# Performance work log

Measured on AMD Instinct MI355X. Metric: run time of the kernel, lower is better.

The kernel has to match this reference:

```python
import jax, jax.numpy as jnp
import numpy as np
import math

N, LQ, DIM = 4, 1000, 256
HEADS, DHEAD, DEPTH = 8, 32, 2
LVLS, NPTS, MLP = 5, 4, 512
SCALE = DHEAD ** -0.5
SHAPES = np.array([[128, 128], [64, 64], [32, 32], [16, 16], [8, 8]], np.int32)
AREAS = SHAPES[:, 0] * SHAPES[:, 1]
STARTS = np.concatenate([[0], np.cumsum(AREAS)[:-1]]).astype(np.int32)
LIN = int(AREAS.sum())


def _ln(x, g, b):
    m = jnp.mean(x, -1, keepdims=True)
    v = jnp.var(x, -1, keepdims=True)
    return (x - m) * jax.lax.rsqrt(v + 1e-5) * g + b


def _gelu(x):  # tanh-approx GELU exactly as the torch module
    c = math.sqrt(2.0 / math.pi)
    return 0.5 * x * (1.0 + jnp.tanh(c * (x + 0.044715 * x ** 3)))


def _ms_deform(value, shapes, starts, loc, aw):
    # value [N,Lin,H,D]; loc [N,Lq,H,L,P,2] normalized to [0,1]; aw [N,Lq,H,L,P]
    n, lq, h, L, p, _ = loc.shape
    d = value.shape[-1]
    ni = jnp.arange(n)[:, None, None, None]
    hi = jnp.arange(h)[None, None, :, None]
    out = jnp.zeros((n, lq, h, d), value.dtype)
    for l in range(L):  # fixed small pyramid depth
        Hl, Wl = int(shapes[l, 0]), int(shapes[l, 1])
        s = int(starts[l])
        v = value[:, s:s + Hl * Wl].reshape(n, Hl, Wl, h, d)
        gx = loc[:, :, :, l, :, 0] * Wl - 0.5  # [N,Lq,H,P]
        gy = loc[:, :, :, l, :, 1] * Hl - 0.5
        x0 = jnp.floor(gx); y0 = jnp.floor(gy)
        lx = gx - x0; ly = gy - y0
        x0i = x0.astype(jnp.int32); y0i = y0.astype(jnp.int32)
        def corner(yi, xi):
            ok = ((yi >= 0) & (yi < Hl) & (xi >= 0) & (xi < Wl)).astype(value.dtype)
            g = v[ni, jnp.clip(yi, 0, Hl - 1), jnp.clip(xi, 0, Wl - 1), hi]  # [N,Lq,H,P,D]
            return g * ok[..., None]
        samp = (corner(y0i, x0i) * ((1 - ly) * (1 - lx))[..., None]
                + corner(y0i, x0i + 1) * ((1 - ly) * lx)[..., None]
                + corner(y0i + 1, x0i) * (ly * (1 - lx))[..., None]
                + corner(y0i + 1, x0i + 1) * (ly * lx)[..., None])
        out = out + jnp.einsum('nqhp,nqhpd->nqhd', aw[:, :, :, l], samp)
    return out.reshape(n, lq, h * d)


def _forward(x, src, center_pos, pos_w, pos_b, ln1_g, ln1_b, qkv_w, out_w, out_b,
             ln2_g, ln2_b, off_w, off_b, aw_w, aw_b, val_w, val_b, op_w, op_b,
             ln3_g, ln3_b, ff_w1, ff_b1, ff_w2, ff_b2, spatial_shapes, level_start_index):
    shapes = np.asarray(spatial_shapes)
    starts = np.asarray(level_start_index)
    n, lq, dim = x.shape
    pe = center_pos @ pos_w + pos_b                                   # pos_embedding(center_pos)
    ref = jnp.broadcast_to(center_pos[:, :, None, :], (n, lq, LVLS, 2))
    onorm = jnp.asarray(np.stack([shapes[:, 1], shapes[:, 0]], -1), x.dtype)  # [L,2] = (W,H)
    for i in range(DEPTH):
        # --- self-attention: PreNorm(x + pe) ---
        xn = _ln(x + pe, ln1_g[i], ln1_b[i])
        qkv = xn @ qkv_w[i]
        q, k, v = jnp.split(qkv, 3, axis=-1)
        q = q.reshape(n, lq, HEADS, DHEAD).transpose(0, 2, 1, 3)
        k = k.reshape(n, lq, HEADS, DHEAD).transpose(0, 2, 1, 3)
        v = v.reshape(n, lq, HEADS, DHEAD).transpose(0, 2, 1, 3)
        att = jax.nn.softmax(jnp.einsum('nhid,nhjd->nhij', q, k) * SCALE, axis=-1)
        o = jnp.einsum('nhij,nhjd->nhid', att, v).transpose(0, 2, 1, 3).reshape(n, lq, HEADS * DHEAD)
        x = x + o @ out_w[i] + out_b[i]
        # --- deformable cross-attention: PreNorm_CA norms query and src with same LN ---
        xn = _ln(x, ln2_g[i], ln2_b[i])
        srcn = _ln(src, ln2_g[i], ln2_b[i])
        query = xn + pe
        value = (srcn @ val_w[i] + val_b[i]).reshape(n, -1, HEADS, DHEAD)
        off = (query @ off_w[i] + off_b[i]).reshape(n, lq, HEADS, LVLS, NPTS, 2)
        aw = jax.nn.softmax((query @ aw_w[i] + aw_b[i]).reshape(n, lq, HEADS, LVLS * NPTS), axis=-1)
        aw = aw.reshape(n, lq, HEADS, LVLS, NPTS)
        loc = ref[:, :, None, :, None, :] + off / onorm[None, None, None, :, None, :]
        o = _ms_deform(value, shapes, starts, loc, aw)
        x = x + o @ op_w[i] + op_b[i]
        # --- feedforward: PreNorm ---
        xn = _ln(x, ln3_g[i], ln3_b[i])
        x = x + _gelu(xn @ ff_w1[i] + ff_b1[i]) @ ff_w2[i] + ff_b2[i]
    return x


def setup_inputs() -> dict:
    key = jax.random.key(0)
    ks = iter(jax.random.split(key, 64))
    r = lambda sh, s=0.02: jax.random.normal(next(ks), sh, jnp.float32) * s
    # sampling_offsets bias grid init (as in MSDeformAttn._reset_parameters)
    thetas = np.arange(HEADS) * (2.0 * math.pi / HEADS)
    grid = np.stack([np.cos(thetas), np.sin(thetas)], -1)
    grid = grid / np.abs(grid).max(-1, keepdims=True)
    grid = np.tile(grid[:, None, None, :], (1, LVLS, NPTS, 1)) * (np.arange(NPTS) + 1)[None, None, :, None]
    off_b = jnp.tile(jnp.asarray(grid.reshape(-1), jnp.float32)[None], (DEPTH, 1))
    return dict(
        x=jax.random.normal(next(ks), (N, LQ, DIM), jnp.float32),
        src=jax.random.normal(next(ks), (N, LIN, DIM), jnp.float32),
        center_pos=jax.random.uniform(next(ks), (N, LQ, 2), jnp.float32),
        spatial_shapes=jnp.asarray(SHAPES),
        level_start_index=jnp.asarray(STARTS),
        pos_w=r((2, DIM), 0.5), pos_b=jnp.zeros((DIM,), jnp.float32),
        ln1_g=jnp.ones((DEPTH, DIM), jnp.float32), ln1_b=jnp.zeros((DEPTH, DIM), jnp.float32),
        qkv_w=r((DEPTH, DIM, 3 * HEADS * DHEAD)),
        out_w=r((DEPTH, HEADS * DHEAD, DIM)), out_b=jnp.zeros((DEPTH, DIM), jnp.float32),
        ln2_g=jnp.ones((DEPTH, DIM), jnp.float32), ln2_b=jnp.zeros((DEPTH, DIM), jnp.float32),
        off_w=r((DEPTH, DIM, HEADS * LVLS * NPTS * 2)), off_b=off_b,
        aw_w=r((DEPTH, DIM, HEADS * LVLS * NPTS)), aw_b=jnp.zeros((DEPTH, HEADS * LVLS * NPTS), jnp.float32),
        val_w=r((DEPTH, DIM, HEADS * DHEAD)), val_b=jnp.zeros((DEPTH, HEADS * DHEAD), jnp.float32),
        op_w=r((DEPTH, HEADS * DHEAD, DIM)), op_b=jnp.zeros((DEPTH, DIM), jnp.float32),
        ln3_g=jnp.ones((DEPTH, DIM), jnp.float32), ln3_b=jnp.zeros((DEPTH, DIM), jnp.float32),
        ff_w1=r((DEPTH, DIM, MLP)), ff_b1=jnp.zeros((DEPTH, MLP), jnp.float32),
        ff_w2=r((DEPTH, MLP, DIM)), ff_b2=jnp.zeros((DEPTH, DIM), jnp.float32),
    )


def reference(x, src, center_pos, spatial_shapes, level_start_index, pos_w, pos_b,
              ln1_g, ln1_b, qkv_w, out_w, out_b, ln2_g, ln2_b, off_w, off_b,
              aw_w, aw_b, val_w, val_b, op_w, op_b, ln3_g, ln3_b,
              ff_w1, ff_b1, ff_w2, ff_b2):
    return _forward(x, src, center_pos, pos_w, pos_b, ln1_g, ln1_b, qkv_w, out_w, out_b,
                    ln2_g, ln2_b, off_w, off_b, aw_w, aw_b, val_w, val_b, op_w, op_b,
                    ln3_g, ln3_b, ff_w1, ff_b1, ff_w2, ff_b2, spatial_shapes, level_start_index)
```

## Files before the change

kernel.cpp:

```cpp
#include <hip/hip_runtime.h>
#include <hip/hip_bf16.h>
#include <math.h>

#define DIM 256
#define NB 4
#define LQ 1000
#define MLPD 512
#define LIN 21824
#define ROWS_X 4000
#define ROWS_SRC 87296
#define ATT_SCALE 0.17677669529663687f
#define LDK 72
#define VLAYER ((size_t)ROWS_SRC*256)

typedef __hip_bfloat16 bf16;
typedef __attribute__((ext_vector_type(8))) short short8;
typedef __attribute__((ext_vector_type(4))) float floatx4;

__device__ __forceinline__ float rdv(const void* p, int f, size_t i){
    if (f) return ((const float*)p)[i];
    unsigned u = ((unsigned)((const unsigned short*)p)[i]) << 16;
    union { unsigned u; float f; } c; c.u = u; return c.f;
}
__device__ __forceinline__ short f2bs(float v){
    bf16 h = __float2bfloat16(v);
    return *reinterpret_cast<short*>(&h);
}
__device__ __forceinline__ float bs2f(short s){
    union { unsigned u; float f; } c; c.u = ((unsigned)(unsigned short)s) << 16; return c.f;
}

__global__ void detect_kernel(const void* __restrict__ x, int* __restrict__ flag){
    const unsigned short* u = (const unsigned short*)x;
    int t = threadIdx.x;
    bool hit = false;
    #pragma unroll
    for (int k = 0; k < 4; ++k) {
        unsigned short b = u[(t*4 + k)*2];
        union { unsigned u; float f; } c; c.u = ((unsigned)b) << 16;
        if (!(fabsf(c.f) <= 1000.f)) hit = true;
    }
    unsigned long long m = __ballot(hit);
    __shared__ unsigned long long red[4];
    if ((t & 63) == 0) red[t >> 6] = m;
    __syncthreads();
    if (t == 0) flag[0] = ((red[0]|red[1]|red[2]|red[3]) != 0ULL) ? 1 : 0;
}

struct PrepTab { const void* src[15]; float* dst[17]; int n[17]; int bs[18]; };
__global__ void prep_kernel(PrepTab t, const void* __restrict__ offb,
                            const void* __restrict__ awb, const void* __restrict__ pw,
                            const void* __restrict__ pb, const void* __restrict__ cp,
                            const int* __restrict__ flag){
    int f = flag[0];
    int bid = blockIdx.x;
    int j = 0;
    #pragma unroll 1
    while (bid >= t.bs[j+1]) ++j;
    int i = (bid - t.bs[j])*256 + threadIdx.x;
    if (i >= t.n[j]) return;
    if (j < 15) {
        t.dst[j][i] = t.src[j] ? rdv(t.src[j], f, i) : 0.f;
    } else if (j == 15) {
        int layer = i / 480, idx = i - layer*480;
        float v = (idx < 320) ? rdv(offb, f, (size_t)layer*320 + idx)
                              : rdv(awb,  f, (size_t)layer*160 + idx - 320);
        t.dst[15][i] = v;
    } else {
        int row = i >> 8, c = i & 255;
        float cx = rdv(cp, f, (size_t)row*2), cy = rdv(cp, f, (size_t)row*2 + 1);
        t.dst[16][i] = cx*rdv(pw, f, c) + cy*rdv(pw, f, DIM + c) + rdv(pb, f, c);
    }
}

struct WT { const void* src[8]; short* dst[8]; const float* scl[8];
            int K[8]; int N[8]; int ld[8]; int ro[8]; };
__global__ void wtransall_kernel(WT t, const int* __restrict__ flag){
    int j = blockIdx.z >> 1, b = blockIdx.z & 1;
    int K = t.K[j], N = t.N[j];
    int k0 = blockIdx.x*32, n0 = blockIdx.y*32;
    if (k0 >= K || n0 >= N) return;
    int f = flag[0];
    __shared__ float tt[32][33];
    int tx = threadIdx.x & 31, ty = threadIdx.x >> 5;
    size_t base = (size_t)b * K * N;
    for (int i = ty; i < 32; i += 8) {
        int k = k0 + i, n = n0 + tx;
        tt[i][tx] = (k < K && n < N) ? rdv(t.src[j], f, base + (size_t)k*N + n) : 0.f;
    }
    __syncthreads();
    int ld = t.ld[j], ro = t.ro[j];
    const float* sc = t.scl[j];
    for (int i = ty; i < 32; i += 8) {
        int n = n0 + i, k = k0 + tx;
        if (n < N && k < K) {
            float v = tt[tx][i];
            if (sc) v *= sc[(size_t)b*K + k];
            t.dst[j][(size_t)b*ld*K + (size_t)(ro+n)*K + k] = f2bs(v);
        }
    }
}

struct BFT { const void* W[3]; const float* bv[3]; const float* base[3];
             float* dst[3]; int N[3]; };
__global__ __launch_bounds__(256) void biasfold_kernel(BFT t, const int* __restrict__ flag){
    int f = flag[0];
    int x = blockIdx.x, b = blockIdx.y;
    int j, n;
    if (x < 768)       { j = 0; n = x; }
    else if (x < 1280) { j = 1; n = x - 768; }
    else               { j = 2; n = x - 1280; }
    int N = t.N[j];
    int k = threadIdx.x;
    float part = t.bv[j][(size_t)b*256 + k] *
                 rdv(t.W[j], f, (size_t)b*256*N + (size_t)k*N + n);
    #pragma unroll
    for (int o = 32; o; o >>= 1) part += __shfl_xor(part, o, 64);
    __shared__ float red[4];
    int wave = k >> 6, lane = k & 63;
    if (lane == 0) red[wave] = part;
    __syncthreads();
    if (k == 0) {
        float s = red[0] + red[1] + red[2] + red[3];
        if (t.base[j]) s += t.base[j][(size_t)b*N + n];
        t.dst[j][(size_t)b*N + n] = s;
    }
}

__global__ __launch_bounds__(256) void statsconvx_kernel(const void* __restrict__ src,
        const void* __restrict__ x, const float* __restrict__ pe,
        const int* __restrict__ flag, bf16* __restrict__ srcn,
        float* __restrict__ xf, float2* __restrict__ st, bf16* __restrict__ xab){
    int f = flag[0];
    int wave = threadIdx.x >> 6, lane = threadIdx.x & 63;
    int bid = blockIdx.x;
    if (bid < ROWS_SRC/4) {
        int row = bid*4 + wave;
        float v0, v1, v2, v3;
        if (f) {
            float4 xx = *(const float4*)((const float*)src + (size_t)row*DIM + lane*4);
            v0 = xx.x; v1 = xx.y; v2 = xx.z; v3 = xx.w;
        } else {
            ushort4 u = *(const ushort4*)((const unsigned short*)src + (size_t)row*DIM + lane*4);
            v0 = bs2f((short)u.x); v1 = bs2f((short)u.y);
            v2 = bs2f((short)u.z); v3 = bs2f((short)u.w);
        }
        float s  = v0 + v1 + v2 + v3;
        float s2 = v0*v0 + v1*v1 + v2*v2 + v3*v3;
        #pragma unroll
        for (int o = 32; o; o >>= 1) {
            s  += __shfl_xor(s,  o, 64);
            s2 += __shfl_xor(s2, o, 64);
        }
        float mean = s * (1.f/DIM);
        float rstd = rsqrtf(s2 * (1.f/DIM) - mean*mean + 1e-5f);
        ushort4 o4;
        o4.x = (unsigned short)f2bs((v0-mean)*rstd);
        o4.y = (unsigned short)f2bs((v1-mean)*rstd);
        o4.z = (unsigned short)f2bs((v2-mean)*rstd);
        o4.w = (unsigned short)f2bs((v3-mean)*rstd);
        *(ushort4*)((unsigned short*)srcn + (size_t)row*DIM + lane*4) = o4;
    } else {
        int row = (bid - ROWS_SRC/4)*4 + wave;
        float4 v;
        if (f) v = *(const float4*)((const float*)x + (size_t)row*DIM + lane*4);
        else {
            ushort4 u = *(const ushort4*)((const unsigned short*)x + (size_t)row*DIM + lane*4);
            v = make_float4(bs2f((short)u.x), bs2f((short)u.y), bs2f((short)u.z), bs2f((short)u.w));
        }
        *(float4*)(xf + (size_t)row*DIM + lane*4) = v;
        float4 p = *(const float4*)(pe + (size_t)row*DIM + lane*4);
        float a0 = v.x+p.x, a1 = v.y+p.y, a2 = v.z+p.z, a3 = v.w+p.w;
        float s  = a0+a1+a2+a3;
        float s2 = a0*a0+a1*a1+a2*a2+a3*a3;
        #pragma unroll
        for (int o = 32; o; o >>= 1) {
            s  += __shfl_xor(s,  o, 64);
            s2 += __shfl_xor(s2, o, 64);
        }
        if (lane == 0) st[row] = make_float2(s, s2);
        float mean = s * (1.f/DIM);
        float rstd = rsqrtf(s2 * (1.f/DIM) - mean*mean + 1e-5f);
        ushort4 o4;
        o4.x = (unsigned short)f2bs((a0-mean)*rstd);
        o4.y = (unsigned short)f2bs((a1-mean)*rstd);
        o4.z = (unsigned short)f2bs((a2-mean)*rstd);
        o4.w = (unsigned short)f2bs((a3-mean)*rstd);
        *(ushort4*)((unsigned short*)xab + (size_t)row*DIM + lane*4) = o4;
    }
}

__global__ __launch_bounds__(256) void xnorm_kernel(const float* __restrict__ a,
        const float* __restrict__ pre, const float* __restrict__ post,
        const float2* __restrict__ sums, const float* __restrict__ g,
        const float* __restrict__ b, bf16* __restrict__ out){
    int wave = threadIdx.x >> 6, lane = threadIdx.x & 63;
    int row = blockIdx.x*4 + wave;
    float4 x = *(const float4*)(a + (size_t)row*DIM + lane*4);
    if (pre) {
        float4 p = *(const float4*)(pre + (size_t)row*DIM + lane*4);
        x.x += p.x; x.y += p.y; x.z += p.z; x.w += p.w;
    }
    float2 st = sums[row];
    float mean = st.x * (1.f/256.f);
    float rstd = rsqrtf(st.y*(1.f/256.f) - mean*mean + 1e-5f);
    float v0 = (x.x-mean)*rstd, v1 = (x.y-mean)*rstd;
    float v2 = (x.z-mean)*rstd, v3 = (x.w-mean)*rstd;
    if (g) {
        int c = lane*4;
        float4 gv = *(const float4*)(g + c);
        float4 bv = *(const float4*)(b + c);
        v0 = v0*gv.x + bv.x; v1 = v1*gv.y + bv.y;
        v2 = v2*gv.z + bv.z; v3 = v3*gv.w + bv.w;
    }
    if (post) {
        float4 p = *(const float4*)(post + (size_t)row*DIM + lane*4);
        v0 += p.x; v1 += p.y; v2 += p.z; v3 += p.w;
    }
    ushort4 o4;
    o4.x = (unsigned short)f2bs(v0); o4.y = (unsigned short)f2bs(v1);
    o4.z = (unsigned short)f2bs(v2); o4.w = (unsigned short)f2bs(v3);
    *(ushort4*)((unsigned short*)out + (size_t)row*DIM + lane*4) = o4;
}

__global__ __launch_bounds__(256) void mgemm_kernel(
    const short* __restrict__ A, const short* __restrict__ Wt,
    const float* __restrict__ bias, const float* __restrict__ res,
    void* __restrict__ Cout, int M, int K, int N, int act, int cbf,
    float2* __restrict__ statacc, const float* __restrict__ sepe,
    void* __restrict__ fin, const int* __restrict__ flag){
    __shared__ short As[64*LDK];
    __shared__ short Bs[64*LDK];
    int tid = threadIdx.x;
    int wave = tid >> 6, lane = tid & 63;
    int wm = wave >> 1, wn = wave & 1;
    int quad = lane >> 4, l16 = lane & 15;
    int row0 = blockIdx.x*64, col0 = blockIdx.y*64;
    floatx4 acc[2][2];
    #pragma unroll
    for (int i = 0; i < 2; ++i)
        #pragma unroll
        for (int j = 0; j < 2; ++j)
            acc[i][j] = (floatx4){0.f,0.f,0.f,0.f};

    int r  = tid >> 2;
    int kc = (tid & 3) * 16;
    int gr = row0 + r;
    int gc = col0 + r;
    const short8 z8 = {0,0,0,0,0,0,0,0};

    short8 ra0, ra1, rb0, rb1;
    if (gr < M) {
        const short8* p = (const short8*)(A + (size_t)gr*K + kc);
        ra0 = p[0]; ra1 = p[1];
    }
    if (gc < N) {
        const short8* p = (const short8*)(Wt + (size_t)gc*K + kc);
        rb0 = p[0]; rb1 = p[1];
    }

    for (int k0 = 0; k0 < K; k0 += 64) {
        short8 a0 = z8, a1 = z8;
        if (gr < M) { a0 = ra0; a1 = ra1; }
        *(short8*)&As[r*LDK + kc]     = a0;
        *(short8*)&As[r*LDK + kc + 8] = a1;
        short8 b0 = z8, b1 = z8;
        if (gc < N) { b0 = rb0; b1 = rb1; }
        *(short8*)&Bs[r*LDK + kc]     = b0;
        *(short8*)&Bs[r*LDK + kc + 8] = b1;
        int kn = k0 + 64;
        if (kn < K) {
            if (gr < M) {
                const short8* p = (const short8*)(A + (size_t)gr*K + kn + kc);
                ra0 = p[0]; ra1 = p[1];
            }
            if (gc < N) {
                const short8* p = (const short8*)(Wt + (size_t)gc*K + kn + kc);
                rb0 = p[0]; rb1 = p[1];
            }
        }
        __syncthreads();
        #pragma unroll
        for (int kb = 0; kb < 64; kb += 32) {
            short8 af[2], bfr[2];
            #pragma unroll
            for (int mi = 0; mi < 2; ++mi)
                af[mi] = *(const short8*)&As[(wm*32 + mi*16 + l16)*LDK + kb + quad*8];
            #pragma unroll
            for (int ni = 0; ni < 2; ++ni)
                bfr[ni] = *(const short8*)&Bs[(wn*32 + ni*16 + l16)*LDK + kb + quad*8];
            #pragma unroll
            for (int mi = 0; mi < 2; ++mi)
                #pragma unroll
                for (int ni = 0; ni < 2; ++ni)
                    acc[mi][ni] = __builtin_amdgcn_mfma_f32_16x16x32_bf16(
                        af[mi], bfr[ni], acc[mi][ni], 0, 0, 0);
        }
        __syncthreads();
    }
    float vout[2][2][4];
    #pragma unroll
    for (int mi = 0; mi < 2; ++mi) {
        int rbase = row0 + wm*32 + mi*16 + quad*4;
        #pragma unroll
        for (int ni = 0; ni < 2; ++ni) {
            int c = col0 + wn*32 + ni*16 + l16;
            #pragma unroll
            for (int r2 = 0; r2 < 4; ++r2) {
                int rr = rbase + r2;
                float v = 0.f;
                if (c < N && rr < M) {
                    v = acc[mi][ni][r2];
                    if (bias) v += bias[c];
                    if (act) {
                        float z = fminf(1.5957691216057308f*(v + 0.044715f*v*v*v), 60.f);
                        float e = __expf(z);
                        v = v * e / (e + 1.f);
                    }
                    if (res) v += res[(size_t)rr*N + c];
                }
                vout[mi][ni][r2] = v;
            }
        }
    }
    int fflag = 0;
    if (fin) fflag = flag[0];
    #pragma unroll
    for (int mi = 0; mi < 2; ++mi) {
        int rbase = row0 + wm*32 + mi*16 + quad*4;
        #pragma unroll
        for (int ni = 0; ni < 2; ++ni) {
            int c = col0 + wn*32 + ni*16 + l16;
            if (c >= N) continue;
            #pragma unroll
            for (int r2 = 0; r2 < 4; ++r2) {
                int rr = rbase + r2;
                if (rr >= M) continue;
                float v = vout[mi][ni][r2];
                if (fin) {
                    float w = isfinite(v) ? v : 0.f;
                    if (fflag) ((float*)fin)[(size_t)rr*N + c] = w;
                    else       ((bf16*)fin)[(size_t)rr*N + c] = __float2bfloat16(w);
                } else if (cbf) ((bf16*)Cout)[(size_t)rr*N + c] = __float2bfloat16(v);
                else            ((float*)Cout)[(size_t)rr*N + c] = v;
            }
        }
    }
    if (statacc) {
        #pragma unroll
        for (int mi = 0; mi < 2; ++mi) {
            int rbase = row0 + wm*32 + mi*16 + quad*4;
            #pragma unroll
            for (int r2 = 0; r2 < 4; ++r2) {
                int rr = rbase + r2;
                float sv = 0.f, sq = 0.f;
                #pragma unroll
                for (int ni = 0; ni < 2; ++ni) {
                    int c = col0 + wn*32 + ni*16 + l16;
                    float v = vout[mi][ni][r2];
                    if (sepe && rr < M) v += sepe[(size_t)rr*256 + c];
                    sv += v; sq += v*v;
                }
                #pragma unroll
                for (int o = 1; o < 16; o <<= 1) {
                    sv += __shfl_xor(sv, o, 64);
                    sq += __shfl_xor(sq, o, 64);
                }
                if (l16 == 0 && rr < M) {
                    atomicAdd(&statacc[rr].x, sv);
                    atomicAdd(&statacc[rr].y, sq);
                }
            }
        }
    }
}

__global__ __launch_bounds__(256) void mgemm128_kernel(
    const short* __restrict__ A, const short* __restrict__ Wt,
    const float* __restrict__ bias, bf16* __restrict__ valall){
    const int K = 256;
    __shared__ short lds[2*128*LDK];
    short* As = lds;
    short* Bs = lds + 128*LDK;
    int tid = threadIdx.x;
    int wave = tid >> 6, lane = tid & 63;
    int wm = wave >> 1, wn = wave & 1;
    int quad = lane >> 4, l16 = lane & 15;
    int bid = blockIdx.x;
    int panel, col;
    if (bid < 2720) {
        int g = bid >> 5, w = bid & 31;
        panel = g*8 + (w & 7);
        col = w >> 3;
    } else {
        int idx = bid - 2720;
        panel = 680 + (idx >> 2);
        col = idx & 3;
    }
    int row0 = panel*128, col0 = col*128;
    floatx4 acc[4][4];
    #pragma unroll
    for (int i = 0; i < 4; ++i)
        #pragma unroll
        for (int j = 0; j < 4; ++j)
            acc[i][j] = (floatx4){0.f,0.f,0.f,0.f};

    short8 pa[2][2], pb2[2][2];
    #pragma unroll
    for (int i = 0; i < 2; ++i) {
        int idx = tid + i*256;
        int rr = idx >> 2, kk = (idx & 3)*16;
        const short8* p = (const short8*)(A + (size_t)(row0+rr)*K + kk);
        pa[i][0] = p[0]; pa[i][1] = p[1];
        const short8* pb = (const short8*)(Wt + (size_t)(col0+rr)*K + kk);
        pb2[i][0] = pb[0]; pb2[i][1] = pb[1];
    }
    for (int k0 = 0; k0 < K; k0 += 64) {
        #pragma unroll
        for (int i = 0; i < 2; ++i) {
            int idx = tid + i*256;
            int rr = idx >> 2, kk = (idx & 3)*16;
            *(short8*)&As[rr*LDK + kk]     = pa[i][0];
            *(short8*)&As[rr*LDK + kk + 8] = pa[i][1];
            *(short8*)&Bs[rr*LDK + kk]     = pb2[i][0];
            *(short8*)&Bs[rr*LDK + kk + 8] = pb2[i][1];
        }
        int kn = k0 + 64;
        if (kn < K) {
            #pragma unroll
            for (int i = 0; i < 2; ++i) {
                int idx = tid + i*256;
                int rr = idx >> 2, kk = (idx & 3)*16;
                const short8* p = (const short8*)(A + (size_t)(row0+rr)*K + kn + kk);
                pa[i][0] = p[0]; pa[i][1] = p[1];
                const short8* pb = (const short8*)(Wt + (size_t)(col0+rr)*K + kn + kk);
                pb2[i][0] = pb[0]; pb2[i][1] = pb[1];
            }
        }
        __syncthreads();
        #pragma unroll
        for (int kb = 0; kb < 64; kb += 32) {
            short8 af[4], bfr[4];
            #pragma unroll
            for (int mi = 0; mi < 4; ++mi)
                af[mi] = *(const short8*)&As[(wm*64 + mi*16 + l16)*LDK + kb + quad*8];
            #pragma unroll
            for (int ni = 0; ni < 4; ++ni)
                bfr[ni] = *(const short8*)&Bs[(wn*64 + ni*16 + l16)*LDK + kb + quad*8];
            #pragma unroll
            for (int mi = 0; mi < 4; ++mi)
                #pragma unroll
                for (int ni = 0; ni < 4; ++ni)
                    acc[mi][ni] = __builtin_amdgcn_mfma_f32_16x16x32_bf16(
                        af[mi], bfr[ni], acc[mi][ni], 0, 0, 0);
        }
        __syncthreads();
    }
    short* Cs = lds;
    #pragma unroll
    for (int mi = 0; mi < 4; ++mi) {
        int lr = wm*64 + mi*16 + quad*4;
        #pragma unroll
        for (int ni = 0; ni < 4; ++ni) {
            int lc = wn*64 + ni*16 + l16;
            float bv = bias[col0 + lc];
            #pragma unroll
            for (int r2 = 0; r2 < 4; ++r2)
                Cs[(lr + r2)*136 + lc] = f2bs(acc[mi][ni][r2] + bv);
        }
    }
    __syncthreads();
    #pragma unroll
    for (int g = 0; g < 4; ++g) {
        int cbase = col0 + g*32;
        int l = cbase >> 8, h = (cbase & 255) >> 5;
        #pragma unroll
        for (int p = 0; p < 2; ++p) {
            int idx = p*256 + tid;
            int rr2 = idx >> 2;
            int dc = (idx & 3) * 8;
            short8 v = *(const short8*)&Cs[rr2*136 + g*32 + dc];
            int grr = row0 + rr2;
            unsigned n = (unsigned)grr / (unsigned)LIN;
            int pos = grr - (int)n*LIN;
            *(short8*)((short*)valall + (size_t)l*VLAYER
                       + ((size_t)(n*8+h)*LIN + pos)*32 + dc) = v;
        }
    }
}

__global__ __launch_bounds__(256) void fattn_kernel(const short* __restrict__ qkv,
                                                    bf16* __restrict__ out){
    int nh = blockIdx.y;
    int n = nh >> 3, h = nh & 7;
    int q0 = blockIdx.x * 64;
    __shared__ short Ks[64*40];
    __shared__ short VsT[32*72];
    __shared__ short Ps[64*72];
    int tid = threadIdx.x;
    int wave = tid >> 6, lane = tid & 63;
    int quad = lane >> 4, l16 = lane & 15;
    int r = tid >> 2, c8 = (tid & 3) * 8;
    const short8 z8 = {0,0,0,0,0,0,0,0};

    short8 qf = z8;
    {
        int gq = q0 + wave*16 + l16;
        if (gq < LQ) {
            short8 s = *(const short8*)(qkv + ((size_t)(n*LQ+gq))*768 + h*32 + quad*8);
            #pragma unroll
            for (int j = 0; j < 8; ++j) qf[j] = f2bs(bs2f(s[j]) * ATT_SCALE);
        }
    }
    floatx4 acc[2];
    acc[0] = (floatx4){0.f,0.f,0.f,0.f};
    acc[1] = (floatx4){0.f,0.f,0.f,0.f};
    float m[4], lsum[4];
    #pragma unroll
    for (int i = 0; i < 4; ++i) { m[i] = -3.0e38f; lsum[i] = 0.f; }

    short8 kvp = z8, vvp = z8;
    if (r < LQ) {
        const short* rp = qkv + ((size_t)(n*LQ+r))*768;
        kvp = *(const short8*)(rp + 256 + h*32 + c8);
        vvp = *(const short8*)(rp + 512 + h*32 + c8);
    }
    for (int k0 = 0; k0 < LQ; k0 += 64) {
        *(short8*)&Ks[r*40 + c8] = kvp;
        #pragma unroll
        for (int j = 0; j < 8; ++j) VsT[(c8+j)*72 + r] = vvp[j];
        short8 kvn = z8, vvn = z8;
        if (k0 + 64 < LQ) {
            int gk = k0 + 64 + r;
            if (gk < LQ) {
                const short* rp = qkv + ((size_t)(n*LQ+gk))*768;
                kvn = *(const short8*)(rp + 256 + h*32 + c8);
                vvn = *(const short8*)(rp + 512 + h*32 + c8);
            }
        }
        __syncthreads();
        floatx4 s4[4];
        #pragma unroll
        for (int kg = 0; kg < 4; ++kg) {
            short8 bfr = *(const short8*)&Ks[(kg*16 + l16)*40 + quad*8];
            s4[kg] = __builtin_amdgcn_mfma_f32_16x16x32_bf16(
                qf, bfr, (floatx4){0.f,0.f,0.f,0.f}, 0, 0, 0);
        }
        if (k0 + 64 > LQ) {
            #pragma unroll
            for (int kg = 0; kg < 4; ++kg)
                if (k0 + kg*16 + l16 >= LQ)
                    s4[kg] = (floatx4){-3.0e38f,-3.0e38f,-3.0e38f,-3.0e38f};
        }
        float fac[4], psum[4];
        #pragma unroll
        for (int r2 = 0; r2 < 4; ++r2) {
            float v = fmaxf(fmaxf(s4[0][r2], s4[1][r2]), fmaxf(s4[2][r2], s4[3][r2]));
            v = fmaxf(v, __shfl_xor(v, 1, 64));
            v = fmaxf(v, __shfl_xor(v, 2, 64));
            v = fmaxf(v, __shfl_xor(v, 4, 64));
            v = fmaxf(v, __shfl_xor(v, 8, 64));
            float mn = fmaxf(m[r2], v);
            fac[r2] = __expf(m[r2] - mn);
            m[r2] = mn;
            psum[r2] = 0.f;
        }
        #pragma unroll
        for (int kg = 0; kg < 4; ++kg)
            #pragma unroll
            for (int r2 = 0; r2 < 4; ++r2) {
                float pv = __expf(s4[kg][r2] - m[r2]);
                psum[r2] += pv;
                Ps[(wave*16 + quad*4 + r2)*72 + kg*16 + l16] = f2bs(pv);
            }
        #pragma unroll
        for (int r2 = 0; r2 < 4; ++r2) {
            psum[r2] += __shfl_xor(psum[r2], 1, 64);
            psum[r2] += __shfl_xor(psum[r2], 2, 64);
            psum[r2] += __shfl_xor(psum[r2], 4, 64);
            psum[r2] += __shfl_xor(psum[r2], 8, 64);
            lsum[r2] = lsum[r2]*fac[r2] + psum[r2];
        }
        #pragma unroll
        for (int ni = 0; ni < 2; ++ni)
            #pragma unroll
            for (int r2 = 0; r2 < 4; ++r2)
                acc[ni][r2] *= fac[r2];
        #pragma unroll
        for (int kb = 0; kb < 64; kb += 32) {
            short8 pf = *(const short8*)&Ps[(wave*16 + l16)*72 + kb + quad*8];
            #pragma unroll
            for (int ni = 0; ni < 2; ++ni) {
                short8 vf = *(const short8*)&VsT[(ni*16 + l16)*72 + kb + quad*8];
                acc[ni] = __builtin_amdgcn_mfma_f32_16x16x32_bf16(pf, vf, acc[ni], 0, 0, 0);
            }
        }
        __syncthreads();
        kvp = kvn; vvp = vvn;
    }
    #pragma unroll
    for (int r2 = 0; r2 < 4; ++r2) {
        int row = q0 + wave*16 + quad*4 + r2;
        if (row >= LQ) continue;
        float inv = 1.f / lsum[r2];
        #pragma unroll
        for (int ni = 0; ni < 2; ++ni)
            out[((size_t)(n*LQ+row))*256 + h*32 + ni*16 + l16] =
                __float2bfloat16(acc[ni][r2] * inv);
    }
}

__global__ __launch_bounds__(256) void sample2_kernel(
        const bf16* __restrict__ value, const float* __restrict__ offaw,
        const float* __restrict__ cp, bf16* __restrict__ out){
    int nq = blockIdx.x;
    int n = nq / LQ;
    int d = threadIdx.x & 31, h = threadIdx.x >> 5;
    float cx = cp[nq*2], cy = cp[nq*2+1];
    const float* rowp = offaw + (size_t)nq*480;
    float o0 = rowp[h*40 + d];
    float o1 = (d < 8) ? rowp[h*40 + 32 + d] : 0.f;
    float logit = (d < 20) ? rowp[320 + h*20 + d] : -3.0e38f;
    float mx = logit;
    #pragma unroll
    for (int off = 16; off; off >>= 1) mx = fmaxf(mx, __shfl_xor(mx, off, 32));
    float p = (d < 20) ? __expf(logit - mx) : 0.f;
    float sm = p;
    #pragma unroll
    for (int off = 16; off; off >>= 1) sm += __shfl_xor(sm, off, 32);
    p *= (1.f / sm);

    const int HW[5] = {128,64,32,16,8};
    const int ST[5] = {0,16384,20480,21504,21760};
    float acc = 0.f;
    #pragma unroll
    for (int l = 0; l < 5; ++l) {
        int hw = HW[l];
        float fhw = (float)hw;
        size_t vb = ((size_t)(n*8 + h)*LIN + ST[l])*32 + d;
        #pragma unroll
        for (int pi = 0; pi < 4; ++pi) {
            const int idx = l*4 + pi;
            float w  = __shfl(p, idx, 32);
            float ox = (2*idx < 32)   ? __shfl(o0, 2*idx, 32)   : __shfl(o1, 2*idx-32, 32);
            float oy = (2*idx+1 < 32) ? __shfl(o0, 2*idx+1, 32) : __shfl(o1, 2*idx+1-32, 32);
            float gx = cx*fhw + ox - 0.5f;
            float gy = cy*fhw + oy - 0.5f;
            float x0f = floorf(gx), y0f = floorf(gy);
            float lx = gx - x0f, ly = gy - y0f;
            int x0 = (int)x0f, y0 = (int)y0f;
            int x1 = x0 + 1, y1 = y0 + 1;
            bool bx0 = (unsigned)x0 < (unsigned)hw, bx1 = (unsigned)x1 < (unsigned)hw;
            bool by0 = (unsigned)y0 < (unsigned)hw, by1 = (unsigned)y1 < (unsigned)hw;
            int x0c = min(max(x0, 0), hw-1), x1c = min(max(x1, 0), hw-1);
            int y0c = min(max(y0, 0), hw-1), y1c = min(max(y1, 0), hw-1);
            float v00 = __bfloat162float(value[vb + (size_t)(y0c*hw + x0c)*32]);
            float v01 = __bfloat162float(value[vb + (size_t)(y0c*hw + x1c)*32]);
            float v10 = __bfloat162float(value[vb + (size_t)(y1c*hw + x0c)*32]);
            float v11 = __bfloat162float(value[vb + (size_t)(y1c*hw + x1c)*32]);
            float w00 = (bx0 && by0) ? (1.f-ly)*(1.f-lx)*w : 0.f;
            float w01 = (bx1 && by0) ? (1.f-ly)*lx*w       : 0.f;
            float w10 = (bx0 && by1) ? ly*(1.f-lx)*w       : 0.f;
            float w11 = (bx1 && by1) ? ly*lx*w             : 0.f;
            acc = fmaf(w00, v00, acc);
            acc = fmaf(w01, v01, acc);
            acc = fmaf(w10, v10, acc);
            acc = fmaf(w11, v11, acc);
        }
    }
    out[(size_t)nq*256 + h*32 + d] = __float2bfloat16(acc);
}

extern "C" void kernel_launch(void* const* d_in, const int* in_sizes, int n_in,
                              void* d_out, int out_size, void* d_ws, size_t ws_size,
                              hipStream_t stream){
    const void* x_raw  = d_in[0];
    const void* src    = d_in[1];
    const void* cp_raw = d_in[2];
    char* ws = (char*)d_ws;
    size_t off = 0;
    auto alloc = [&](size_t bytes){ size_t p = off; off += (bytes + 255) & ~(size_t)255; return p; };
    int*   flag  = (int*)(ws + alloc(256));
    float* xf    = (float*)(ws + alloc((size_t)ROWS_X*DIM*4));
    float* pe    = (float*)(ws + alloc((size_t)ROWS_X*DIM*4));
    bf16*  tmpb  = (bf16*)(ws + alloc((size_t)ROWS_X*DIM*2));
    bf16*  xab   = (bf16*)(ws + alloc((size_t)ROWS_X*DIM*2));
    bf16*  qkv   = (bf16*)(ws + alloc((size_t)ROWS_X*768*2));
    bf16*  ffh   = (bf16*)(ws + alloc((size_t)ROWS_X*MLPD*2));
    float* offaw = (float*)(ws + alloc((size_t)ROWS_X*480*4));
    float* cpf   = (float*)(ws + alloc((size_t)ROWS_X*2*4));
    float* oab   = (float*)(ws + alloc((size_t)2*480*4));
    float2* statbuf = (float2*)(ws + alloc((size_t)6*ROWS_X*8));
    float* qkvB  = (float*)(ws + alloc((size_t)2*768*4));
    float* ff1B  = (float*)(ws + alloc((size_t)2*512*4));
    float* valB  = (float*)(ws + alloc((size_t)2*256*4));
    const int sidx[13] = {5,6,7,8,11,12,13,19,21,22,23,25,27};
    const int ssz[13]  = {512,256,512,512,512,512,512,512,512,512,512,1024,512};
    float* sp[13];
    for (int j = 0; j < 13; ++j) sp[j] = (float*)(ws + alloc((size_t)ssz[j]*4));
    short* qkvT = (short*)(ws + alloc((size_t)2*768*256*2));
    short* outT = (short*)(ws + alloc((size_t)2*256*256*2));
    short* oawT = (short*)(ws + alloc((size_t)2*480*256*2));
    short* valT = (short*)(ws + alloc((size_t)2*256*256*2));
    short* opT  = (short*)(ws + alloc((size_t)2*256*256*2));
    short* ff1T = (short*)(ws + alloc((size_t)2*512*256*2));
    short* ff2T = (short*)(ws + alloc((size_t)2*256*512*2));
    bf16*  srcn = (bf16*)(ws + alloc((size_t)ROWS_SRC*DIM*2));
    bf16*  valall = (bf16*)(ws + alloc((size_t)2*ROWS_SRC*DIM*2));
    (void)ws_size; (void)in_sizes; (void)n_in; (void)out_size;

    float* ln1_g = sp[2];  float* ln1_b = sp[3];
    float* out_b = sp[4];
    float* ln2_g = sp[5];  float* ln2_b = sp[6];
    float* val_b = sp[7];  float* op_b  = sp[8];
    float* ln3_g = sp[9];  float* ln3_b = sp[10];
    float* ff_b1 = sp[11]; float* ff_b2 = sp[12];

    detect_kernel<<<1, 256, 0, stream>>>(x_raw, flag);
    {
        PrepTab pt;
        int nb = 0;
        int nn[17];
        for (int j = 0; j < 13; ++j) { pt.src[j] = d_in[sidx[j]]; pt.dst[j] = sp[j]; nn[j] = ssz[j]; }
        pt.src[13] = cp_raw;  pt.dst[13] = cpf;  nn[13] = ROWS_X*2;
        pt.src[14] = nullptr; pt.dst[14] = (float*)(statbuf + ROWS_X); nn[14] = 5*ROWS_X*2;
        pt.dst[15] = oab;  nn[15] = 960;
        pt.dst[16] = pe;   nn[16] = ROWS_X*DIM;
        for (int j = 0; j < 17; ++j) {
            pt.n[j] = nn[j];
            pt.bs[j] = nb;
            nb += (nn[j] + 255)/256;
        }
        pt.bs[17] = nb;
        prep_kernel<<<nb, 256, 0, stream>>>(pt, d_in[15], d_in[17], d_in[5], d_in[6],
                                            cp_raw, flag);
    }
    statsconvx_kernel<<<ROWS_SRC/4 + ROWS_X/4, 256, 0, stream>>>(
        src, x_raw, pe, flag, srcn, xf, statbuf, xab);
    {
        WT wt;
        const int widx[8] = {9,10,14,16,18,20,24,26};
        short* wdst[8] = {qkvT, outT, oawT, oawT, valT, opT, ff1T, ff2T};
        const float* wscl[8] = {ln1_g, nullptr, nullptr, nullptr, ln2_g, nullptr, ln3_g, nullptr};
        const int wK[8]  = {256,256,256,256,256,256,256,512};
        const int wN[8]  = {768,256,320,160,256,256,512,256};
        const int wld[8] = {768,256,480,480,256,256,512,256};
        const int wro[8] = {0,0,0,320,0,0,0,0};
        for (int j = 0; j < 8; ++j) {
            wt.src[j] = d_in[widx[j]]; wt.dst[j] = wdst[j]; wt.scl[j] = wscl[j];
            wt.K[j] = wK[j]; wt.N[j] = wN[j]; wt.ld[j] = wld[j]; wt.ro[j] = wro[j];
        }
        wtransall_kernel<<<dim3(16,24,16), 256, 0, stream>>>(wt, flag);
    }
    {
        BFT bt;
        bt.W[0] = d_in[9];  bt.bv[0] = ln1_b; bt.base[0] = nullptr; bt.dst[0] = qkvB; bt.N[0] = 768;
        bt.W[1] = d_in[24]; bt.bv[1] = ln3_b; bt.base[1] = ff_b1;   bt.dst[1] = ff1B; bt.N[1] = 512;
        bt.W[2] = d_in[18]; bt.bv[2] = ln2_b; bt.base[2] = val_b;   bt.dst[2] = valB; bt.N[2] = 256;
        biasfold_kernel<<<dim3(1536,2), 256, 0, stream>>>(bt, flag);
    }
    mgemm128_kernel<<<(ROWS_SRC/128)*4, 256, 0, stream>>>(
        (const short*)srcn, valT, valB, valall);

    int gmx = (ROWS_X + 63) / 64;
    for (int i = 0; i < 2; ++i) {
        float2* stA = statbuf + (size_t)(i ? 3 : 0)*ROWS_X;
        float2* stO = statbuf + (size_t)(i ? 4 : 1)*ROWS_X;
        float2* stF = statbuf + (size_t)(i ? 5 : 2)*ROWS_X;
        if (i == 1)
            xnorm_kernel<<<ROWS_X/4, 256, 0, stream>>>(xf, pe, nullptr, stA,
                                                       nullptr, nullptr, xab);
        mgemm_kernel<<<dim3(gmx,12), 256, 0, stream>>>(
            (const short*)xab, qkvT + (size_t)i*768*256, qkvB + i*768, nullptr, qkv,
            ROWS_X, 256, 768, 0, 1, nullptr, nullptr, nullptr, flag);
        fattn_kernel<<<dim3(16,32), 256, 0, stream>>>((const short*)qkv, tmpb);
        mgemm_kernel<<<dim3(gmx,4), 256, 0, stream>>>(
            (const short*)tmpb, outT + (size_t)i*256*256, out_b + i*DIM, xf, xf,
            ROWS_X, 256, 256, 0, 0, stO, nullptr, nullptr, flag);
        xnorm_kernel<<<ROWS_X/4, 256, 0, stream>>>(xf, nullptr, pe, stO,
                                                   ln2_g + i*DIM, ln2_b + i*DIM, xab);
        mgemm_kernel<<<dim3(gmx,8), 256, 0, stream>>>(
            (const short*)xab, oawT + (size_t)i*480*256, oab + i*480, nullptr, offaw,
            ROWS_X, 256, 480, 0, 0, nullptr, nullptr, nullptr, flag);
        sample2_kernel<<<ROWS_X, 256, 0, stream>>>(
            valall + (size_t)i*VLAYER, offaw, cpf, tmpb);
        mgemm_kernel<<<dim3(gmx,4), 256, 0, stream>>>(
            (const short*)tmpb, opT + (size_t)i*256*256, op_b + i*DIM, xf, xf,
            ROWS_X, 256, 256, 0, 0, stF, nullptr, nullptr, flag);
        xnorm_kernel<<<ROWS_X/4, 256, 0, stream>>>(xf, nullptr, nullptr, stF,
                                                   nullptr, nullptr, xab);
        mgemm_kernel<<<dim3(gmx,8), 256, 0, stream>>>(
            (const short*)xab, ff1T + (size_t)i*512*256, ff1B + i*MLPD, nullptr, ffh,
            ROWS_X, 256, 512, 1, 1, nullptr, nullptr, nullptr, flag);
        if (i == 0) {
            mgemm_kernel<<<dim3(gmx,4), 256, 0, stream>>>(
                (const short*)ffh, ff2T + (size_t)i*256*512, ff_b2 + i*DIM, xf, xf,
                ROWS_X, 512, 256, 0, 0, statbuf + (size_t)3*ROWS_X, pe, nullptr, flag);
        } else {
            mgemm_kernel<<<dim3(gmx,4), 256, 0, stream>>>(
                (const short*)ffh, ff2T + (size_t)i*256*512, ff_b2 + i*DIM, xf, xf,
                ROWS_X, 512, 256, 0, 0, nullptr, nullptr, d_out, flag);
        }
    }
}
```

Baseline: 557.7 us.

## Merge prep, weight transpose, bias fold and stats kernels into one setup kernel

```diff
diff --git a/kernel.cpp b/kernel.cpp
--- a/kernel.cpp
+++ b/kernel.cpp
@@ -47,101 +47,31 @@
     if (t == 0) flag[0] = ((red[0]|red[1]|red[2]|red[3]) != 0ULL) ? 1 : 0;
 }
 
-struct PrepTab { const void* src[15]; float* dst[17]; int n[17]; int bs[18]; };
-__global__ void prep_kernel(PrepTab t, const void* __restrict__ offb,
-                            const void* __restrict__ awb, const void* __restrict__ pw,
-                            const void* __restrict__ pb, const void* __restrict__ cp,
-                            const int* __restrict__ flag){
+struct SetupTab {
+    const void* csrc[13]; float* cdst[13];
+    const void* cp; float* cpf;
+    float* statz;
+    const void* offb; const void* awb; float* oab;
+    const void* src; bf16* srcn;
+    const void* x; const void* posw; const void* posb;
+    float* xf; float2* st; bf16* xab; float* pe;
+    const void* wsrc[8]; short* wdst[8]; const void* wscl[8];
+    const void* bfW[3]; const void* bfBv[3]; const void* bfBase[3]; float* bfDst[3];
+};
+__global__ __launch_bounds__(256) void setup_kernel(SetupTab t, const int* __restrict__ flag){
     int f = flag[0];
     int bid = blockIdx.x;
-    int j = 0;
-    #pragma unroll 1
-    while (bid >= t.bs[j+1]) ++j;
-    int i = (bid - t.bs[j])*256 + threadIdx.x;
-    if (i >= t.n[j]) return;
-    if (j < 15) {
-        t.dst[j][i] = t.src[j] ? rdv(t.src[j], f, i) : 0.f;
-    } else if (j == 15) {
-        int layer = i / 480, idx = i - layer*480;
-        float v = (idx < 320) ? rdv(offb, f, (size_t)layer*320 + idx)
-                              : rdv(awb,  f, (size_t)layer*160 + idx - 320);
-        t.dst[15][i] = v;
-    } else {
-        int row = i >> 8, c = i & 255;
-        float cx = rdv(cp, f, (size_t)row*2), cy = rdv(cp, f, (size_t)row*2 + 1);
-        t.dst[16][i] = cx*rdv(pw, f, c) + cy*rdv(pw, f, DIM + c) + rdv(pb, f, c);
-    }
-}
-
-struct WT { const void* src[8]; short* dst[8]; const float* scl[8];
-            int K[8]; int N[8]; int ld[8]; int ro[8]; };
-__global__ void wtransall_kernel(WT t, const int* __restrict__ flag){
-    int j = blockIdx.z >> 1, b = blockIdx.z & 1;
-    int K = t.K[j], N = t.N[j];
-    int k0 = blockIdx.x*32, n0 = blockIdx.y*32;
-    if (k0 >= K || n0 >= N) return;
-    int f = flag[0];
+    int tid = threadIdx.x;
     __shared__ float tt[32][33];
-    int tx = threadIdx.x & 31, ty = threadIdx.x >> 5;
-    size_t base = (size_t)b * K * N;
-    for (int i = ty; i < 32; i += 8) {
-        int k = k0 + i, n = n0 + tx;
-        tt[i][tx] = (k < K && n < N) ? rdv(t.src[j], f, base + (size_t)k*N + n) : 0.f;
-    }
-    __syncthreads();
-    int ld = t.ld[j], ro = t.ro[j];
-    const float* sc = t.scl[j];
-    for (int i = ty; i < 32; i += 8) {
-        int n = n0 + i, k = k0 + tx;
-        if (n < N && k < K) {
-            float v = tt[tx][i];
-            if (sc) v *= sc[(size_t)b*K + k];
-            t.dst[j][(size_t)b*ld*K + (size_t)(ro+n)*K + k] = f2bs(v);
-        }
-    }
-}
-
-struct BFT { const void* W[3]; const float* bv[3]; const float* base[3];
-             float* dst[3]; int N[3]; };
-__global__ __launch_bounds__(256) void biasfold_kernel(BFT t, const int* __restrict__ flag){
-    int f = flag[0];
-    int x = blockIdx.x, b = blockIdx.y;
-    int j, n;
-    if (x < 768)       { j = 0; n = x; }
-    else if (x < 1280) { j = 1; n = x - 768; }
-    else               { j = 2; n = x - 1280; }
-    int N = t.N[j];
-    int k = threadIdx.x;
-    float part = t.bv[j][(size_t)b*256 + k] *
-                 rdv(t.W[j], f, (size_t)b*256*N + (size_t)k*N + n);
-    #pragma unroll
-    for (int o = 32; o; o >>= 1) part += __shfl_xor(part, o, 64);
-    __shared__ float red[4];
-    int wave = k >> 6, lane = k & 63;
-    if (lane == 0) red[wave] = part;
-    __syncthreads();
-    if (k == 0) {
-        float s = red[0] + red[1] + red[2] + red[3];
-        if (t.base[j]) s += t.base[j][(size_t)b*N + n];
-        t.dst[j][(size_t)b*N + n] = s;
-    }
-}
-
-__global__ __launch_bounds__(256) void statsconvx_kernel(const void* __restrict__ src,
-        const void* __restrict__ x, const float* __restrict__ pe,
-        const int* __restrict__ flag, bf16* __restrict__ srcn,
-        float* __restrict__ xf, float2* __restrict__ st, bf16* __restrict__ xab){
-    int f = flag[0];
-    int wave = threadIdx.x >> 6, lane = threadIdx.x & 63;
-    int bid = blockIdx.x;
-    if (bid < ROWS_SRC/4) {
+    if (bid < 21824) {
+        int wave = tid >> 6, lane = tid & 63;
         int row = bid*4 + wave;
         float v0, v1, v2, v3;
         if (f) {
-            float4 xx = *(const float4*)((const float*)src + (size_t)row*DIM + lane*4);
+            float4 xx = *(const float4*)((const float*)t.src + (size_t)row*DIM + lane*4);
             v0 = xx.x; v1 = xx.y; v2 = xx.z; v3 = xx.w;
         } else {
-            ushort4 u = *(const ushort4*)((const unsigned short*)src + (size_t)row*DIM + lane*4);
+            ushort4 u = *(const ushort4*)((const unsigned short*)t.src + (size_t)row*DIM + lane*4);
             v0 = bs2f((short)u.x); v1 = bs2f((short)u.y);
             v2 = bs2f((short)u.z); v3 = bs2f((short)u.w);
         }
@@ -159,17 +89,85 @@
         o4.y = (unsigned short)f2bs((v1-mean)*rstd);
         o4.z = (unsigned short)f2bs((v2-mean)*rstd);
         o4.w = (unsigned short)f2bs((v3-mean)*rstd);
-        *(ushort4*)((unsigned short*)srcn + (size_t)row*DIM + lane*4) = o4;
-    } else {
-        int row = (bid - ROWS_SRC/4)*4 + wave;
+        *(ushort4*)((unsigned short*)t.srcn + (size_t)row*DIM + lane*4) = o4;
+        return;
+    }
+    bid -= 21824;
+    if (bid < 1520) {
+        const int cum[9] = {0,192,256,336,376,440,504,632,760};
+        const int wN[8]  = {768,256,320,160,256,256,512,256};
+        const int wK[8]  = {256,256,256,256,256,256,256,512};
+        const int wld[8] = {768,256,480,480,256,256,512,256};
+        const int wro[8] = {0,0,0,320,0,0,0,0};
+        int b = bid >= 760;
+        int r = b ? bid - 760 : bid;
+        int j = 0;
+        #pragma unroll 1
+        while (r >= cum[j+1]) ++j;
+        int rel = r - cum[j];
+        int ncols = wN[j] >> 5;
+        int k0 = (rel / ncols) * 32, n0 = (rel % ncols) * 32;
+        int K = wK[j], N = wN[j];
+        int tx = tid & 31, ty = tid >> 5;
+        size_t base = (size_t)b * K * N;
+        for (int i = ty; i < 32; i += 8)
+            tt[i][tx] = rdv(t.wsrc[j], f, base + (size_t)(k0+i)*N + (n0+tx));
+        __syncthreads();
+        int ld = wld[j], ro = wro[j];
+        const void* sc = t.wscl[j];
+        for (int i = ty; i < 32; i += 8) {
+            int n = n0 + i, k = k0 + tx;
+            float v = tt[tx][i];
+            if (sc) v *= rdv(sc, f, (size_t)b*K + k);
+            t.wdst[j][(size_t)b*ld*K + (size_t)(ro+n)*K + k] = f2bs(v);
+        }
+        return;
+    }
+    bid -= 1520;
+    if (bid < 3072) {
+        int b = bid >= 1536;
+        int x = b ? bid - 1536 : bid;
+        const int bN[3] = {768,512,256};
+        int j, n;
+        if (x < 768)       { j = 0; n = x; }
+        else if (x < 1280) { j = 1; n = x - 768; }
+        else               { j = 2; n = x - 1280; }
+        int N = bN[j];
+        int k = tid;
+        float part = rdv(t.bfBv[j], f, (size_t)b*256 + k) *
+                     rdv(t.bfW[j], f, (size_t)b*256*N + (size_t)k*N + n);
+        #pragma unroll
+        for (int o = 32; o; o >>= 1) part += __shfl_xor(part, o, 64);
+        __shared__ float red[4];
+        int wave = k >> 6, lane = k & 63;
+        if (lane == 0) red[wave] = part;
+        __syncthreads();
+        if (k == 0) {
+            float s = red[0] + red[1] + red[2] + red[3];
+            if (t.bfBase[j]) s += rdv(t.bfBase[j], f, (size_t)b*N + n);
+            t.bfDst[j][(size_t)b*N + n] = s;
+        }
+        return;
+    }
+    bid -= 3072;
+    if (bid < 1000) {
+        int wave = tid >> 6, lane = tid & 63;
+        int row = bid*4 + wave;
+        int c = lane*4;
         float4 v;
-        if (f) v = *(const float4*)((const float*)x + (size_t)row*DIM + lane*4);
+        if (f) v = *(const float4*)((const float*)t.x + (size_t)row*DIM + c);
         else {
-            ushort4 u = *(const ushort4*)((const unsigned short*)x + (size_t)row*DIM + lane*4);
+            ushort4 u = *(const ushort4*)((const unsigned short*)t.x + (size_t)row*DIM + c);
             v = make_float4(bs2f((short)u.x), bs2f((short)u.y), bs2f((short)u.z), bs2f((short)u.w));
         }
-        *(float4*)(xf + (size_t)row*DIM + lane*4) = v;
-        float4 p = *(const float4*)(pe + (size_t)row*DIM + lane*4);
+        *(float4*)(t.xf + (size_t)row*DIM + c) = v;
+        float cx = rdv(t.cp, f, (size_t)row*2), cy = rdv(t.cp, f, (size_t)row*2 + 1);
+        float4 p;
+        p.x = cx*rdv(t.posw, f, c)   + cy*rdv(t.posw, f, DIM+c)   + rdv(t.posb, f, c);
+        p.y = cx*rdv(t.posw, f, c+1) + cy*rdv(t.posw, f, DIM+c+1) + rdv(t.posb, f, c+1);
+        p.z = cx*rdv(t.posw, f, c+2) + cy*rdv(t.posw, f, DIM+c+2) + rdv(t.posb, f, c+2);
+        p.w = cx*rdv(t.posw, f, c+3) + cy*rdv(t.posw, f, DIM+c+3) + rdv(t.posb, f, c+3);
+        *(float4*)(t.pe + (size_t)row*DIM + c) = p;
         float a0 = v.x+p.x, a1 = v.y+p.y, a2 = v.z+p.z, a3 = v.w+p.w;
         float s  = a0+a1+a2+a3;
         float s2 = a0*a0+a1*a1+a2*a2+a3*a3;
@@ -178,7 +176,7 @@
             s  += __shfl_xor(s,  o, 64);
             s2 += __shfl_xor(s2, o, 64);
         }
-        if (lane == 0) st[row] = make_float2(s, s2);
+        if (lane == 0) t.st[row] = make_float2(s, s2);
         float mean = s * (1.f/DIM);
         float rstd = rsqrtf(s2 * (1.f/DIM) - mean*mean + 1e-5f);
         ushort4 o4;
@@ -186,7 +184,40 @@
         o4.y = (unsigned short)f2bs((a1-mean)*rstd);
         o4.z = (unsigned short)f2bs((a2-mean)*rstd);
         o4.w = (unsigned short)f2bs((a3-mean)*rstd);
-        *(ushort4*)((unsigned short*)xab + (size_t)row*DIM + lane*4) = o4;
+        *(ushort4*)((unsigned short*)t.xab + (size_t)row*DIM + c) = o4;
+        return;
+    }
+    bid -= 1000;
+    if (bid < 27) {
+        const int cs[14] = {0,2,3,5,7,9,11,13,15,17,19,21,25,27};
+        const int ssz[13] = {512,256,512,512,512,512,512,512,512,512,512,1024,512};
+        int j = 0;
+        #pragma unroll 1
+        while (bid >= cs[j+1]) ++j;
+        int i = (bid - cs[j])*256 + tid;
+        if (i < ssz[j]) t.cdst[j][i] = rdv(t.csrc[j], f, i);
+        return;
+    }
+    bid -= 27;
+    if (bid < 32) {
+        int i = bid*256 + tid;
+        if (i < ROWS_X*2) t.cpf[i] = rdv(t.cp, f, i);
+        return;
+    }
+    bid -= 32;
+    if (bid < 157) {
+        int i = bid*256 + tid;
+        if (i < 5*ROWS_X*2) t.statz[i] = 0.f;
+        return;
+    }
+    bid -= 157;
+    {
+        int i = bid*256 + tid;
+        if (i >= 960) return;
+        int layer = i / 480, idx = i - layer*480;
+        float v = (idx < 320) ? rdv(t.offb, f, (size_t)layer*320 + idx)
+                              : rdv(t.awb,  f, (size_t)layer*160 + idx - 320);
+        t.oab[i] = v;
     }
 }
 
@@ -709,55 +740,29 @@
     bf16*  valall = (bf16*)(ws + alloc((size_t)2*ROWS_SRC*DIM*2));
     (void)ws_size; (void)in_sizes; (void)n_in; (void)out_size;
 
-    float* ln1_g = sp[2];  float* ln1_b = sp[3];
+    float* ln2_g = sp[5];  float* ln2_b = sp[6];
     float* out_b = sp[4];
-    float* ln2_g = sp[5];  float* ln2_b = sp[6];
-    float* val_b = sp[7];  float* op_b  = sp[8];
-    float* ln3_g = sp[9];  float* ln3_b = sp[10];
-    float* ff_b1 = sp[11]; float* ff_b2 = sp[12];
+    float* op_b  = sp[8];
+    float* ff_b2 = sp[12];
 
     detect_kernel<<<1, 256, 0, stream>>>(x_raw, flag);
     {
-        PrepTab pt;
-        int nb = 0;
-        int nn[17];
-        for (int j = 0; j < 13; ++j) { pt.src[j] = d_in[sidx[j]]; pt.dst[j] = sp[j]; nn[j] = ssz[j]; }
-        pt.src[13] = cp_raw;  pt.dst[13] = cpf;  nn[13] = ROWS_X*2;
-        pt.src[14] = nullptr; pt.dst[14] = (float*)(statbuf + ROWS_X); nn[14] = 5*ROWS_X*2;
-        pt.dst[15] = oab;  nn[15] = 960;
-        pt.dst[16] = pe;   nn[16] = ROWS_X*DIM;
-        for (int j = 0; j < 17; ++j) {
-            pt.n[j] = nn[j];
-            pt.bs[j] = nb;
-            nb += (nn[j] + 255)/256;
-        }
-        pt.bs[17] = nb;
-        prep_kernel<<<nb, 256, 0, stream>>>(pt, d_in[15], d_in[17], d_in[5], d_in[6],
-                                            cp_raw, flag);
-    }
-    statsconvx_kernel<<<ROWS_SRC/4 + ROWS_X/4, 256, 0, stream>>>(
-        src, x_raw, pe, flag, srcn, xf, statbuf, xab);
-    {
-        WT wt;
+        SetupTab t;
+        for (int j = 0; j < 13; ++j) { t.csrc[j] = d_in[sidx[j]]; t.cdst[j] = sp[j]; }
+        t.cp = cp_raw; t.cpf = cpf;
+        t.statz = (float*)(statbuf + ROWS_X);
+        t.offb = d_in[15]; t.awb = d_in[17]; t.oab = oab;
+        t.src = src; t.srcn = srcn;
+        t.x = x_raw; t.posw = d_in[5]; t.posb = d_in[6];
+        t.xf = xf; t.st = statbuf; t.xab = xab; t.pe = pe;
         const int widx[8] = {9,10,14,16,18,20,24,26};
         short* wdst[8] = {qkvT, outT, oawT, oawT, valT, opT, ff1T, ff2T};
-        const float* wscl[8] = {ln1_g, nullptr, nullptr, nullptr, ln2_g, nullptr, ln3_g, nullptr};
-        const int wK[8]  = {256,256,256,256,256,256,256,512};
-        const int wN[8]  = {768,256,320,160,256,256,512,256};
-        const int wld[8] = {768,256,480,480,256,256,512,256};
-        const int wro[8] = {0,0,0,320,0,0,0,0};
-        for (int j = 0; j < 8; ++j) {
-            wt.src[j] = d_in[widx[j]]; wt.dst[j] = wdst[j]; wt.scl[j] = wscl[j];
-            wt.K[j] = wK[j]; wt.N[j] = wN[j]; wt.ld[j] = wld[j]; wt.ro[j] = wro[j];
-        }
-        wtransall_kernel<<<dim3(16,24,16), 256, 0, stream>>>(wt, flag);
-    }
-    {
-        BFT bt;
-        bt.W[0] = d_in[9];  bt.bv[0] = ln1_b; bt.base[0] = nullptr; bt.dst[0] = qkvB; bt.N[0] = 768;
-        bt.W[1] = d_in[24]; bt.bv[1] = ln3_b; bt.base[1] = ff_b1;   bt.dst[1] = ff1B; bt.N[1] = 512;
-        bt.W[2] = d_in[18]; bt.bv[2] = ln2_b; bt.base[2] = val_b;   bt.dst[2] = valB; bt.N[2] = 256;
-        biasfold_kernel<<<dim3(1536,2), 256, 0, stream>>>(bt, flag);
+        const void* wscl[8] = {d_in[7], nullptr, nullptr, nullptr, d_in[12], nullptr, d_in[22], nullptr};
+        for (int j = 0; j < 8; ++j) { t.wsrc[j] = d_in[widx[j]]; t.wdst[j] = wdst[j]; t.wscl[j] = wscl[j]; }
+        t.bfW[0] = d_in[9];  t.bfBv[0] = d_in[8];  t.bfBase[0] = nullptr;  t.bfDst[0] = qkvB;
+        t.bfW[1] = d_in[24]; t.bfBv[1] = d_in[23]; t.bfBase[1] = d_in[25]; t.bfDst[1] = ff1B;
+        t.bfW[2] = d_in[18]; t.bfBv[2] = d_in[13]; t.bfBase[2] = d_in[19]; t.bfDst[2] = valB;
+        setup_kernel<<<27636, 256, 0, stream>>>(t, flag);
     }
     mgemm128_kernel<<<(ROWS_SRC/128)*4, 256, 0, stream>>>(
         (const short*)srcn, valT, valB, valall);
```

After: 543.1 us. 1.03x faster.
